# Kernel optimization log

Hardware: AMD Instinct MI355X
Metric: run time of the kernel (lower is better)

The kernel has to match this reference:

```python
import jax, jax.numpy as jnp
import numpy as np

B, S, HID = 2, 2048, 2048
H, KV, D = 16, 8, 128          # query heads, kv heads, head dim
NREP = H // KV
EPS = 1e-6
THETA = 1000000.0
SCALE = 1.0 / np.sqrt(D)


def setup_inputs() -> dict:
    key = jax.random.key(0)
    ks = jax.random.split(key, 5)
    x = jax.random.normal(ks[0], (B, S, HID), jnp.float32)
    std = 0.02
    Wq = jax.random.normal(ks[1], (HID, H * D), jnp.float32) * std
    Wk = jax.random.normal(ks[2], (HID, KV * D), jnp.float32) * std
    Wv = jax.random.normal(ks[3], (HID, KV * D), jnp.float32) * std
    Wo = jax.random.normal(ks[4], (H * D, HID), jnp.float32) * std
    q_norm_w = jnp.ones((D,), jnp.float32)
    k_norm_w = jnp.ones((D,), jnp.float32)
    # standard RoPE cos/sin table: [S, D]
    inv_freq = 1.0 / (THETA ** (jnp.arange(0, D, 2, dtype=jnp.float32) / D))
    freqs = jnp.arange(S, dtype=jnp.float32)[:, None] * inv_freq[None, :]
    emb = jnp.concatenate([freqs, freqs], axis=-1)
    return {"x": x, "Wq": Wq, "Wk": Wk, "Wv": Wv, "Wo": Wo,
            "q_norm_w": q_norm_w, "k_norm_w": k_norm_w,
            "cos": jnp.cos(emb), "sin": jnp.sin(emb)}


def _rmsnorm(x, w, eps=EPS):
    var = jnp.mean(jnp.square(x), axis=-1, keepdims=True)
    return w * (x * jax.lax.rsqrt(var + eps))


def _rotate_half(x):
    x1, x2 = jnp.split(x, 2, axis=-1)
    return jnp.concatenate([-x2, x1], axis=-1)


def _rope(t, cos, sin):
    # t: [B, h, S, D]; cos/sin: [S, D]
    return t * cos[None, None] + _rotate_half(t) * sin[None, None]


def reference(x, Wq, Wk, Wv, Wo, q_norm_w, k_norm_w, cos, sin):
    q = (x @ Wq).reshape(B, S, H, D)
    k = (x @ Wk).reshape(B, S, KV, D)
    v = (x @ Wv).reshape(B, S, KV, D)
    q = _rmsnorm(q, q_norm_w).transpose(0, 2, 1, 3)   # [B, H, S, D]
    k = _rmsnorm(k, k_norm_w).transpose(0, 2, 1, 3)   # [B, KV, S, D]
    v = v.transpose(0, 2, 1, 3)                       # [B, KV, S, D]
    q = _rope(q, cos, sin)
    k = _rope(k, cos, sin)
    # GQA without materializing repeated K/V: group q heads per kv head
    qg = q.reshape(B, KV, NREP, S, D)
    scores = jnp.einsum('bgrsd,bgtd->bgrst', qg, k) * SCALE  # [B,KV,NREP,S,S]
    causal = jnp.tril(jnp.ones((S, S), dtype=bool))
    scores = jnp.where(causal, scores, jnp.finfo(scores.dtype).min)
    p = jax.nn.softmax(scores, axis=-1)
    out = jnp.einsum('bgrst,bgtd->bgrsd', p, v).reshape(B, H, S, D)
    out = out.transpose(0, 2, 1, 3).reshape(B, S, H * D)
    return out @ Wo
```

## Files before the change

kernel.cpp:

```cpp
#include <hip/hip_runtime.h>

typedef unsigned short u16;
typedef __bf16 bf16x8 __attribute__((ext_vector_type(8)));
typedef float f32x4 __attribute__((ext_vector_type(4)));

#define Bn 2
#define Sn 2048
#define HIDn 2048
#define Hn 16
#define KVn 8
#define Dn 128
#define SCALEf 0.08838834764831845f

__device__ __forceinline__ float b2f(u16 v) {
  return __builtin_bit_cast(float, (unsigned)v << 16);
}
__device__ __forceinline__ u16 f2b(float f) {
  unsigned u = __builtin_bit_cast(unsigned, f);
  u += 0x7fffu + ((u >> 16) & 1u);
  return (u16)(u >> 16);
}
__device__ __forceinline__ bool is_bf16(const void* det) {
  return *(const unsigned*)det == 0x3F803F80u;
}
__device__ __forceinline__ float ldx(const void* p, long i, bool isbf) {
  return isbf ? b2f(((const u16*)p)[i]) : ((const float*)p)[i];
}
__device__ __forceinline__ void gl_lds16(const u16* g, u16* l) {
  __builtin_amdgcn_global_load_lds(
      (unsigned int __attribute__((address_space(1)))*)g,
      (unsigned int __attribute__((address_space(3)))*)l, 16, 0, 0);
}

template <int CTRL>
__device__ __forceinline__ float dpp_mov(float x) {
  return __builtin_bit_cast(
      float, __builtin_amdgcn_update_dpp(0, __builtin_bit_cast(int, x), CTRL,
                                         0xF, 0xF, true));
}
__device__ __forceinline__ float red16_max(float x) {
  x = fmaxf(x, dpp_mov<0xB1>(x));
  x = fmaxf(x, dpp_mov<0x4E>(x));
  x = fmaxf(x, dpp_mov<0x141>(x));
  x = fmaxf(x, dpp_mov<0x140>(x));
  return x;
}
__device__ __forceinline__ float red16_sum(float x) {
  x += dpp_mov<0xB1>(x);
  x += dpp_mov<0x4E>(x);
  x += dpp_mov<0x141>(x);
  x += dpp_mov<0x140>(x);
  return x;
}

__global__ __launch_bounds__(256) void convert_x(
    const void* __restrict__ in, u16* __restrict__ out, const void* __restrict__ det) {
  bool isbf = is_bf16(det);
  long i = ((long)blockIdx.x * 256 + threadIdx.x) * 4;
  if (isbf) {
    *(ushort4*)(out + i) = *(const ushort4*)((const u16*)in + i);
  } else {
    float4 f = *(const float4*)((const float*)in + i);
    out[i] = f2b(f.x); out[i + 1] = f2b(f.y); out[i + 2] = f2b(f.z); out[i + 3] = f2b(f.w);
  }
}

__global__ __launch_bounds__(256) void transpose_any(
    const void* __restrict__ vin, u16* __restrict__ out, const void* __restrict__ det,
    int irs, int ors, long ib0, long ob0, int nb1, long ib1, long ob1) {
  __shared__ u16 tile[64][65];
  bool isbf = det ? is_bf16(det) : true;
  int bz = blockIdx.z;
  long ibase = (long)(bz / nb1) * ib0 + (long)(bz % nb1) * ib1;
  u16* op = out + (long)(bz / nb1) * ob0 + (long)(bz % nb1) * ob1;
  long r0 = (long)blockIdx.y * 64, c0 = (long)blockIdx.x * 64;
  int t = threadIdx.x;
  int tr = t >> 3, tc = (t & 7) * 8;
#pragma unroll
  for (int p = 0; p < 2; ++p) {
    int r = p * 32 + tr;
    long src = ibase + (r0 + r) * irs + c0 + tc;
    if (isbf) {
      const u16* ip = (const u16*)vin;
#pragma unroll
      for (int j = 0; j < 8; ++j) tile[r][tc + j] = ip[src + j];
    } else {
      const float* ip = (const float*)vin;
#pragma unroll
      for (int j = 0; j < 8; ++j) tile[r][tc + j] = f2b(ip[src + j]);
    }
  }
  __syncthreads();
#pragma unroll
  for (int p = 0; p < 2; ++p) {
    int r = p * 32 + tr;
    u16* dst = op + (c0 + r) * ors + r0 + tc;
#pragma unroll
    for (int j = 0; j < 8; ++j) dst[j] = tile[tc + j][r];
  }
}

__global__ __launch_bounds__(256) void gemm_bt(
    const u16* __restrict__ A, const u16* __restrict__ Bt, u16* __restrict__ C,
    float* __restrict__ Cf, const void* __restrict__ det, int N, int K) {
  __shared__ alignas(16) u16 As[128 * 64];
  __shared__ alignas(16) u16 Bs[128 * 64];
  int t = threadIdx.x;
  int wave = t >> 6, lane = t & 63, quad = lane >> 4, l15 = lane & 15;
  long bm = (long)blockIdx.y * 128, bn = (long)blockIdx.x * 128;
  int wm = (wave >> 1) * 64, wn = (wave & 1) * 64;
  f32x4 acc[4][4] = {};
  int sg = ((t & 7) ^ ((t >> 3) & 7)) * 8;
  const u16* Ab = A + (bm + (t >> 3)) * K + sg;
  const u16* Bb = Bt + (bn + (t >> 3)) * K + sg;
  for (int k0 = 0; k0 < K; k0 += 64) {
    __syncthreads();
#pragma unroll
    for (int p = 0; p < 4; ++p) {
      gl_lds16(Ab + (long)(p * 32) * K + k0, As + p * 2048 + t * 8);
      gl_lds16(Bb + (long)(p * 32) * K + k0, Bs + p * 2048 + t * 8);
    }
    __syncthreads();
#pragma unroll
    for (int kt = 0; kt < 2; ++kt) {
      int fg = ((kt * 4 + quad) ^ (l15 & 7)) * 8;
      bf16x8 a[4], b[4];
#pragma unroll
      for (int i = 0; i < 4; ++i)
        a[i] = *(const bf16x8*)(As + (wm + i * 16 + l15) * 64 + fg);
#pragma unroll
      for (int j = 0; j < 4; ++j)
        b[j] = *(const bf16x8*)(Bs + (wn + j * 16 + l15) * 64 + fg);
#pragma unroll
      for (int i = 0; i < 4; ++i)
#pragma unroll
        for (int j = 0; j < 4; ++j)
          acc[i][j] = __builtin_amdgcn_mfma_f32_16x16x32_bf16(a[i], b[j], acc[i][j], 0, 0, 0);
    }
  }
  bool tofloat = (Cf != nullptr) && !is_bf16(det);
#pragma unroll
  for (int i = 0; i < 4; ++i) {
    long row = bm + wm + i * 16 + quad * 4;
#pragma unroll
    for (int j = 0; j < 4; ++j) {
      long col = bn + wn + j * 16 + l15;
      if (tofloat) {
#pragma unroll
        for (int r = 0; r < 4; ++r) Cf[(row + r) * N + col] = acc[i][j][r];
      } else {
#pragma unroll
        for (int r = 0; r < 4; ++r) C[(row + r) * N + col] = f2b(acc[i][j][r]);
      }
    }
  }
}

__global__ __launch_bounds__(256) void gemm_qkv(
    const u16* __restrict__ A, const u16* __restrict__ Bt,
    u16* __restrict__ Qout, u16* __restrict__ Kout, u16* __restrict__ Vout,
    int hq, int hk,
    const void* __restrict__ qw, const void* __restrict__ kw,
    const void* __restrict__ cosb, const void* __restrict__ sinb, int K) {
  __shared__ alignas(16) u16 As[128 * 64];
  __shared__ alignas(16) u16 Bs[128 * 64];
  bool isbf = is_bf16(qw);
  int t = threadIdx.x;
  int wave = t >> 6, lane = t & 63, quad = lane >> 4, l15 = lane & 15;
  long bm = (long)blockIdx.y * 128;
  int h = blockIdx.x;
  long bn = (long)h * 128;
  int wm = wave * 32;
  f32x4 acc[2][8] = {};
  int sg = ((t & 7) ^ ((t >> 3) & 7)) * 8;
  const u16* Ab = A + (bm + (t >> 3)) * K + sg;
  const u16* Bb = Bt + (bn + (t >> 3)) * K + sg;
  for (int k0 = 0; k0 < K; k0 += 64) {
    __syncthreads();
#pragma unroll
    for (int p = 0; p < 4; ++p) {
      gl_lds16(Ab + (long)(p * 32) * K + k0, As + p * 2048 + t * 8);
      gl_lds16(Bb + (long)(p * 32) * K + k0, Bs + p * 2048 + t * 8);
    }
    __syncthreads();
#pragma unroll
    for (int kt = 0; kt < 2; ++kt) {
      int fg = ((kt * 4 + quad) ^ (l15 & 7)) * 8;
      bf16x8 a[2], b[8];
#pragma unroll
      for (int i = 0; i < 2; ++i)
        a[i] = *(const bf16x8*)(As + (wm + i * 16 + l15) * 64 + fg);
#pragma unroll
      for (int j = 0; j < 8; ++j)
        b[j] = *(const bf16x8*)(Bs + (j * 16 + l15) * 64 + fg);
#pragma unroll
      for (int i = 0; i < 2; ++i)
#pragma unroll
        for (int j = 0; j < 8; ++j)
          acc[i][j] = __builtin_amdgcn_mfma_f32_16x16x32_bf16(a[i], b[j], acc[i][j], 0, 0, 0);
    }
  }
  if (h < hq + hk) {
    bool isq = h < hq;
    const void* w = isq ? qw : kw;
    int nh = isq ? Hn : KVn;
    int hh = isq ? h : (h - hq);
    u16* Obase = isq ? Qout : Kout;
#pragma unroll
    for (int i = 0; i < 2; ++i) {
#pragma unroll
      for (int r = 0; r < 4; ++r) {
        float ss = 0.f;
#pragma unroll
        for (int j = 0; j < 8; ++j) { float v = acc[i][j][r]; ss += v * v; }
        ss = red16_sum(ss);
        float scale = rsqrtf(ss * (1.0f / 128.0f) + 1e-6f);
        int m = (int)bm + wm + i * 16 + quad * 4 + r;
        int b = m >> 11, s = m & (Sn - 1);
        u16* dst = Obase + (((long)b * nh + hh) * Sn + s) * Dn;
        long cb = (long)s * Dn;
#pragma unroll
        for (int j = 0; j < 4; ++j) {
          int c1i = j * 16 + l15, c2i = c1i + 64;
          float x1 = acc[i][j][r] * scale * ldx(w, c1i, isbf);
          float x2 = acc[i][j + 4][r] * scale * ldx(w, c2i, isbf);
          float c1 = ldx(cosb, cb + c1i, isbf), s1 = ldx(sinb, cb + c1i, isbf);
          float c2 = ldx(cosb, cb + c2i, isbf), s2 = ldx(sinb, cb + c2i, isbf);
          dst[c1i] = f2b(x1 * c1 - x2 * s1);
          dst[c2i] = f2b(x2 * c2 + x1 * s2);
        }
      }
    }
  } else {
    int kv = h - hq - hk;
    int bidx = (int)(bm >> 11);
    int srow = ((int)bm & (Sn - 1)) + wm + quad * 4;
#pragma unroll
    for (int i = 0; i < 2; ++i) {
      int s0 = srow + i * 16;
#pragma unroll
      for (int j = 0; j < 8; ++j) {
        int d = j * 16 + l15;
        ushort4 tmp;
        tmp.x = f2b(acc[i][j][0]);
        tmp.y = f2b(acc[i][j][1]);
        tmp.z = f2b(acc[i][j][2]);
        tmp.w = f2b(acc[i][j][3]);
        *(ushort4*)(Vout + (((long)bidx * KVn + kv) * Dn + d) * Sn + s0) = tmp;
      }
    }
  }
}

__global__ __launch_bounds__(512) void attn_kernel(
    const u16* __restrict__ Qr, const u16* __restrict__ Kr,
    const u16* __restrict__ Vt, u16* __restrict__ Aout) {
  __shared__ alignas(16) u16 Ks[64 * 128];
  __shared__ alignas(16) u16 Vs[128 * 64];
  __shared__ alignas(16) u16 Ps[8][16 * 64];
  int t = threadIdx.x, wave = t >> 6, lane = t & 63, quad = lane >> 4, l15 = lane & 15;
  int bh = blockIdx.y, b = bh >> 4, h = bh & 15, kvh = h >> 1;
  const u16* kbase = Kr + ((long)b * KVn + kvh) * Sn * Dn;
  const u16* vbase = Vt + ((long)b * KVn + kvh) * (long)Dn * Sn;
  int krow = t >> 4;
  int kgr = ((t & 15) ^ (krow & 15)) * 8;
  int vrow = t >> 3;
  int vgr = ((t & 7) ^ (vrow & 7)) * 8;
  u16* ps = (u16*)Ps[wave];

  for (int half = 0; half < 2; ++half) {
    int qt = half == 0 ? (int)blockIdx.x : 15 - (int)blockIdx.x;
    int row0 = qt * 128 + wave * 16;
    const u16* qbase = Qr + (((long)b * Hn + h) * Sn + row0) * Dn;
    bf16x8 aq[4];
#pragma unroll
    for (int kt = 0; kt < 4; ++kt)
      aq[kt] = *(const bf16x8*)(qbase + l15 * Dn + kt * 32 + quad * 8);
    f32x4 o[8] = {};
    float mi[4], li[4];
#pragma unroll
    for (int r = 0; r < 4; ++r) { mi[r] = -1e30f; li[r] = 0.f; }
    int kv_end = qt * 128 + 128;
    for (int kv0 = 0; kv0 < kv_end; kv0 += 64) {
      __syncthreads();
      {
        const u16* kg = kbase + ((long)kv0 + krow) * Dn + kgr;
        gl_lds16(kg, Ks + t * 8);
        gl_lds16(kg + (long)32 * Dn, Ks + 4096 + t * 8);
        const u16* vg = vbase + (long)vrow * Sn + kv0 + vgr;
        gl_lds16(vg, Vs + t * 8);
        gl_lds16(vg + (long)64 * Sn, Vs + 4096 + t * 8);
      }
      __syncthreads();
      if (kv0 <= row0 + 15) {
        f32x4 sc[4] = {};
#pragma unroll
        for (int kt = 0; kt < 4; ++kt) {
          bf16x8 bk[4];
#pragma unroll
          for (int n = 0; n < 4; ++n)
            bk[n] = *(const bf16x8*)(Ks + (n * 16 + l15) * 128 + (((kt * 4 + quad) ^ l15) * 8));
#pragma unroll
          for (int n = 0; n < 4; ++n)
            sc[n] = __builtin_amdgcn_mfma_f32_16x16x32_bf16(aq[kt], bk[n], sc[n], 0, 0, 0);
        }
        f32x4 sv[4];
#pragma unroll
        for (int n = 0; n < 4; ++n)
#pragma unroll
          for (int r = 0; r < 4; ++r) sv[n][r] = sc[n][r] * SCALEf;
        if (kv0 + 63 > row0) {
#pragma unroll
          for (int n = 0; n < 4; ++n) {
            int col = kv0 + n * 16 + l15;
#pragma unroll
            for (int r = 0; r < 4; ++r)
              if (col > row0 + quad * 4 + r) sv[n][r] = -1e30f;
          }
        }
        float alpha[4], pr[4][4];
#pragma unroll
        for (int r = 0; r < 4; ++r) {
          float mx = fmaxf(fmaxf(sv[0][r], sv[1][r]), fmaxf(sv[2][r], sv[3][r]));
          mx = red16_max(mx);
          float mnew = fmaxf(mi[r], mx);
          alpha[r] = __expf(mi[r] - mnew);
          mi[r] = mnew;
          float rs = 0.f;
#pragma unroll
          for (int n = 0; n < 4; ++n) {
            float pv = __expf(sv[n][r] - mnew);
            pr[r][n] = pv;
            rs += pv;
          }
          rs = red16_sum(rs);
          li[r] = li[r] * alpha[r] + rs;
        }
#pragma unroll
        for (int n = 0; n < 8; ++n)
#pragma unroll
          for (int r = 0; r < 4; ++r) o[n][r] *= alpha[r];
#pragma unroll
        for (int n = 0; n < 4; ++n)
#pragma unroll
          for (int r = 0; r < 4; ++r) {
            int prow = quad * 4 + r;
            int pg = (n * 2 + (l15 >> 3)) ^ (prow & 7);
            ps[prow * 64 + pg * 8 + (l15 & 7)] = f2b(pr[r][n]);
          }
#pragma unroll
        for (int kt2 = 0; kt2 < 2; ++kt2) {
          bf16x8 ap = *(const bf16x8*)(ps + l15 * 64 + (((kt2 * 4 + quad) ^ (l15 & 7)) * 8));
#pragma unroll
          for (int n = 0; n < 8; ++n) {
            bf16x8 bv = *(const bf16x8*)(Vs + (n * 16 + l15) * 64 + (((kt2 * 4 + quad) ^ (l15 & 7)) * 8));
            o[n] = __builtin_amdgcn_mfma_f32_16x16x32_bf16(ap, bv, o[n], 0, 0, 0);
          }
        }
      }
    }
#pragma unroll
    for (int r = 0; r < 4; ++r) {
      long s = row0 + quad * 4 + r;
      float inv = 1.0f / li[r];
      u16* dst = Aout + (((long)b * Sn + s) * Hn + h) * Dn;
#pragma unroll
      for (int n = 0; n < 8; ++n) dst[n * 16 + l15] = f2b(o[n][r] * inv);
    }
  }
}

extern "C" void kernel_launch(void* const* d_in, const int* in_sizes, int n_in,
                              void* d_out, int out_size, void* d_ws, size_t ws_size,
                              hipStream_t stream) {
  (void)in_sizes; (void)n_in; (void)out_size;
  const void* x    = d_in[0];
  const void* Wq   = d_in[1];
  const void* Wk   = d_in[2];
  const void* Wv   = d_in[3];
  const void* Wo   = d_in[4];
  const void* qw   = d_in[5];
  const void* kw   = d_in[6];
  const void* cosb = d_in[7];
  const void* sinb = d_in[8];
  u16* ws = (u16*)d_ws;
  u16* dsc = (u16*)d_out;

  u16* Qr = dsc + 0;
  u16* Kr = dsc + 8388608;
  u16* xb = ws + 0;
  dim3 blk(256);
  convert_x<<<dim3(8192), blk, 0, stream>>>(x, xb, qw);

  if (ws_size >= (size_t)33554432) {
    u16* WT = ws + 8388608;
    u16* Vt = dsc + 12582912;
    transpose_any<<<dim3(32, 32, 1), blk, 0, stream>>>(Wq, WT, qw, 2048, 2048, 0, 0, 1, 0, 0);
    transpose_any<<<dim3(16, 32, 1), blk, 0, stream>>>(Wk, WT + (long)2048 * 2048, qw, 1024, 2048, 0, 0, 1, 0, 0);
    transpose_any<<<dim3(16, 32, 1), blk, 0, stream>>>(Wv, WT + (long)3072 * 2048, qw, 1024, 2048, 0, 0, 1, 0, 0);
    gemm_qkv<<<dim3(32, 32), blk, 0, stream>>>(xb, WT, Qr, Kr, Vt, Hn, KVn,
                                               qw, kw, cosb, sinb, 2048);
    u16* attn = ws + 0;
    attn_kernel<<<dim3(8, 32), dim3(512), 0, stream>>>(Qr, Kr, Vt, attn);
    u16* WoT = ws + 8388608;
    transpose_any<<<dim3(32, 32, 1), blk, 0, stream>>>(Wo, WoT, qw, 2048, 2048, 0, 0, 1, 0, 0);
    gemm_bt<<<dim3(16, 32), blk, 0, stream>>>(attn, WoT, (u16*)d_out, (float*)d_out, qw, 2048, 2048);
  } else {
    u16* Wslot = dsc + 12582912;
    u16* Vt    = ws + 8388608;
    transpose_any<<<dim3(32, 32, 1), blk, 0, stream>>>(Wq, Wslot, qw, 2048, 2048, 0, 0, 1, 0, 0);
    gemm_qkv<<<dim3(16, 32), blk, 0, stream>>>(xb, Wslot, Qr, nullptr, nullptr, Hn, 0,
                                               qw, kw, cosb, sinb, 2048);
    transpose_any<<<dim3(16, 32, 1), blk, 0, stream>>>(Wk, Wslot, qw, 1024, 2048, 0, 0, 1, 0, 0);
    transpose_any<<<dim3(16, 32, 1), blk, 0, stream>>>(Wv, Wslot + (long)1024 * 2048, qw, 1024, 2048, 0, 0, 1, 0, 0);
    gemm_qkv<<<dim3(16, 32), blk, 0, stream>>>(xb, Wslot, nullptr, Kr, Vt, 0, KVn,
                                               qw, kw, cosb, sinb, 2048);
    u16* attn = ws + 0;
    attn_kernel<<<dim3(8, 32), dim3(512), 0, stream>>>(Qr, Kr, Vt, attn);
    u16* WoT = ws + 8388608;
    transpose_any<<<dim3(32, 32, 1), blk, 0, stream>>>(Wo, WoT, qw, 2048, 2048, 0, 0, 1, 0, 0);
    gemm_bt<<<dim3(16, 32), blk, 0, stream>>>(attn, WoT, (u16*)d_out, (float*)d_out, qw, 2048, 2048);
  }
}
```

Baseline: 371.3 us.

## Rewrite QKV GEMM as 256x256 tile with double-buffered LDS pipeline

Replaces the 128x128, 256-thread QKV projection GEMM with a 256x256-tile, 512-thread kernel. It double-buffers A and B tiles in LDS, issues next-tile global loads between MFMA phases, and raises wave priority around MFMA bursts. The aim is to raise data reuse per tile and hide global-load latency behind compute. It uses far more LDS and registers per block and launches only 256 blocks, which risks occupancy and CU balance. The small-workspace fallback path is removed, so the kernel now assumes the workspace is large enough.

Result: faster. 360.9 us (-2.8%).

```diff
diff --git a/kernel.cpp b/kernel.cpp
--- a/kernel.cpp
+++ b/kernel.cpp
@@ -156,74 +156,146 @@
   }
 }
 
-__global__ __launch_bounds__(256) void gemm_qkv(
+__global__ __launch_bounds__(512, 2) void gemm_qkv256(
     const u16* __restrict__ A, const u16* __restrict__ Bt,
     u16* __restrict__ Qout, u16* __restrict__ Kout, u16* __restrict__ Vout,
-    int hq, int hk,
     const void* __restrict__ qw, const void* __restrict__ kw,
     const void* __restrict__ cosb, const void* __restrict__ sinb, int K) {
-  __shared__ alignas(16) u16 As[128 * 64];
-  __shared__ alignas(16) u16 Bs[128 * 64];
+  __shared__ alignas(16) u16 As[2][2][8192];
+  __shared__ alignas(16) u16 Bs[2][2][8192];
+  const int NT = K >> 6;
   bool isbf = is_bf16(qw);
   int t = threadIdx.x;
   int wave = t >> 6, lane = t & 63, quad = lane >> 4, l15 = lane & 15;
-  long bm = (long)blockIdx.y * 128;
-  int h = blockIdx.x;
-  long bn = (long)h * 128;
-  int wm = wave * 32;
-  f32x4 acc[2][8] = {};
-  int sg = ((t & 7) ^ ((t >> 3) & 7)) * 8;
-  const u16* Ab = A + (bm + (t >> 3)) * K + sg;
-  const u16* Bb = Bt + (bn + (t >> 3)) * K + sg;
-  for (int k0 = 0; k0 < K; k0 += 64) {
-    __syncthreads();
-#pragma unroll
-    for (int p = 0; p < 4; ++p) {
-      gl_lds16(Ab + (long)(p * 32) * K + k0, As + p * 2048 + t * 8);
-      gl_lds16(Bb + (long)(p * 32) * K + k0, Bs + p * 2048 + t * 8);
-    }
-    __syncthreads();
-#pragma unroll
-    for (int kt = 0; kt < 2; ++kt) {
-      int fg = ((kt * 4 + quad) ^ (l15 & 7)) * 8;
-      bf16x8 a[2], b[8];
-#pragma unroll
-      for (int i = 0; i < 2; ++i)
-        a[i] = *(const bf16x8*)(As + (wm + i * 16 + l15) * 64 + fg);
-#pragma unroll
-      for (int j = 0; j < 8; ++j)
-        b[j] = *(const bf16x8*)(Bs + (j * 16 + l15) * 64 + fg);
-#pragma unroll
-      for (int i = 0; i < 2; ++i)
-#pragma unroll
-        for (int j = 0; j < 8; ++j)
-          acc[i][j] = __builtin_amdgcn_mfma_f32_16x16x32_bf16(a[i], b[j], acc[i][j], 0, 0, 0);
-    }
-  }
-  if (h < hq + hk) {
-    bool isq = h < hq;
+  int l7 = l15 & 7;
+  int wmi = wave >> 1, wni = wave & 1;
+  long bm = (long)blockIdx.y * 256;
+  long bn = (long)blockIdx.x * 256;
+  int s0 = t, s1 = t + 512;
+  int r0 = s0 >> 3, r1 = s1 >> 3;
+  int gs0 = (s0 & 7) ^ (r0 & 7), gs1 = (s1 & 7) ^ (r1 & 7);
+  const u16* Ab0 = A + bm * K;
+  const u16* Ab1 = A + (bm + 128) * K;
+  const u16* Bb0 = Bt + bn * K;
+  const u16* Bb1 = Bt + (bn + 128) * K;
+#define STG(dst, src)                                          \
+  gl_lds16((src) + (long)r0 * K + gs0 * 8, (dst) + s0 * 8);    \
+  gl_lds16((src) + (long)r1 * K + gs1 * 8, (dst) + s1 * 8);
+#define FENCE asm volatile("" ::: "memory")
+  int ah = wmi >> 1;
+  int arb = (wmi & 1) * 64 + l15;
+#define LDA(m, kk) (*(const bf16x8*)(Ah + (arb + (m)*16) * 64 + ((((kk)*4 + quad) ^ l7) * 8)))
+#define LDB(n, kk) (*(const bf16x8*)(Bh + ((n)*16 + l15) * 64 + ((((kk)*4 + quad) ^ l7) * 8)))
+  f32x4 acc[4][8] = {};
+  STG((u16*)As[0][0], Ab0);
+  STG((u16*)As[0][1], Ab1);
+  STG((u16*)Bs[0][0], Bb0);
+  STG((u16*)Bs[0][1], Bb1);
+  STG((u16*)As[1][0], Ab0 + 64);
+  STG((u16*)As[1][1], Ab1 + 64);
+  asm volatile("s_waitcnt vmcnt(4)" ::: "memory");
+  __builtin_amdgcn_s_barrier();
+
+  for (int tk = 0; tk < NT; ++tk) {
+    const u16* Ah = (const u16*)As[tk & 1][ah];
+    const u16* Bh = (const u16*)Bs[tk & 1][wni];
+    u16* BsN0 = (u16*)Bs[(tk + 1) & 1][0];
+    u16* BsN1 = (u16*)Bs[(tk + 1) & 1][1];
+    u16* AsN0 = (u16*)As[tk & 1][0];
+    u16* AsN1 = (u16*)As[tk & 1][1];
+    bf16x8 aa[4], bb[4];
+#pragma unroll
+    for (int m = 0; m < 4; ++m) aa[m] = LDA(m, 0);
+#pragma unroll
+    for (int j = 0; j < 4; ++j) bb[j] = LDB(j, 0);
+    if (tk + 1 < NT) { STG(BsN0, Bb0 + (tk + 1) * 64); }
+    FENCE; __builtin_amdgcn_s_barrier();
+    asm volatile("s_waitcnt lgkmcnt(0)" ::: "memory");
+    __builtin_amdgcn_s_setprio(1);
+#pragma unroll
+    for (int m = 0; m < 4; ++m)
+#pragma unroll
+      for (int j = 0; j < 4; ++j)
+        acc[m][j] = __builtin_amdgcn_mfma_f32_16x16x32_bf16(aa[m], bb[j], acc[m][j], 0, 0, 0);
+    __builtin_amdgcn_s_setprio(0);
+    FENCE; __builtin_amdgcn_s_barrier();
+#pragma unroll
+    for (int j = 0; j < 4; ++j) bb[j] = LDB(j + 4, 0);
+    if (tk + 1 < NT) { STG(BsN1, Bb1 + (tk + 1) * 64); }
+    FENCE; __builtin_amdgcn_s_barrier();
+    asm volatile("s_waitcnt lgkmcnt(0)" ::: "memory");
+    __builtin_amdgcn_s_setprio(1);
+#pragma unroll
+    for (int m = 0; m < 4; ++m)
+#pragma unroll
+      for (int j = 0; j < 4; ++j)
+        acc[m][j + 4] = __builtin_amdgcn_mfma_f32_16x16x32_bf16(aa[m], bb[j], acc[m][j + 4], 0, 0, 0);
+    __builtin_amdgcn_s_setprio(0);
+    FENCE; __builtin_amdgcn_s_barrier();
+#pragma unroll
+    for (int m = 0; m < 4; ++m) aa[m] = LDA(m, 1);
+#pragma unroll
+    for (int j = 0; j < 4; ++j) bb[j] = LDB(j, 1);
+    FENCE; __builtin_amdgcn_s_barrier();
+    asm volatile("s_waitcnt lgkmcnt(0)" ::: "memory");
+    __builtin_amdgcn_s_setprio(1);
+#pragma unroll
+    for (int m = 0; m < 4; ++m)
+#pragma unroll
+      for (int j = 0; j < 4; ++j)
+        acc[m][j] = __builtin_amdgcn_mfma_f32_16x16x32_bf16(aa[m], bb[j], acc[m][j], 0, 0, 0);
+    __builtin_amdgcn_s_setprio(0);
+    FENCE; __builtin_amdgcn_s_barrier();
+#pragma unroll
+    for (int j = 0; j < 4; ++j) bb[j] = LDB(j + 4, 1);
+    if (tk + 2 < NT) {
+      STG(AsN0, Ab0 + (tk + 2) * 64);
+      STG(AsN1, Ab1 + (tk + 2) * 64);
+      asm volatile("s_waitcnt vmcnt(4)" ::: "memory");
+    } else {
+      asm volatile("s_waitcnt vmcnt(0)" ::: "memory");
+    }
+    __builtin_amdgcn_s_barrier();
+    asm volatile("s_waitcnt lgkmcnt(0)" ::: "memory");
+    __builtin_amdgcn_s_setprio(1);
+#pragma unroll
+    for (int m = 0; m < 4; ++m)
+#pragma unroll
+      for (int j = 0; j < 4; ++j)
+        acc[m][j + 4] = __builtin_amdgcn_mfma_f32_16x16x32_bf16(aa[m], bb[j], acc[m][j + 4], 0, 0, 0);
+    __builtin_amdgcn_s_setprio(0);
+    FENCE; __builtin_amdgcn_s_barrier();
+  }
+#undef STG
+#undef LDA
+#undef LDB
+#undef FENCE
+  int hglob = (int)(bn >> 7) + wni;
+  int mrow0 = (int)bm + wmi * 64 + quad * 4;
+  if (hglob < Hn + KVn) {
+    bool isq = hglob < Hn;
     const void* w = isq ? qw : kw;
     int nh = isq ? Hn : KVn;
-    int hh = isq ? h : (h - hq);
-    u16* Obase = isq ? Qout : Kout;
-#pragma unroll
-    for (int i = 0; i < 2; ++i) {
+    int hh = isq ? hglob : hglob - Hn;
+    u16* Ob = isq ? Qout : Kout;
+#pragma unroll
+    for (int m = 0; m < 4; ++m) {
 #pragma unroll
       for (int r = 0; r < 4; ++r) {
         float ss = 0.f;
 #pragma unroll
-        for (int j = 0; j < 8; ++j) { float v = acc[i][j][r]; ss += v * v; }
+        for (int j = 0; j < 8; ++j) { float v = acc[m][j][r]; ss += v * v; }
         ss = red16_sum(ss);
         float scale = rsqrtf(ss * (1.0f / 128.0f) + 1e-6f);
-        int m = (int)bm + wm + i * 16 + quad * 4 + r;
-        int b = m >> 11, s = m & (Sn - 1);
-        u16* dst = Obase + (((long)b * nh + hh) * Sn + s) * Dn;
+        int mr = mrow0 + m * 16 + r;
+        int b = mr >> 11, s = mr & (Sn - 1);
+        u16* dst = Ob + (((long)b * nh + hh) * Sn + s) * Dn;
         long cb = (long)s * Dn;
 #pragma unroll
         for (int j = 0; j < 4; ++j) {
           int c1i = j * 16 + l15, c2i = c1i + 64;
-          float x1 = acc[i][j][r] * scale * ldx(w, c1i, isbf);
-          float x2 = acc[i][j + 4][r] * scale * ldx(w, c2i, isbf);
+          float x1 = acc[m][j][r] * scale * ldx(w, c1i, isbf);
+          float x2 = acc[m][j + 4][r] * scale * ldx(w, c2i, isbf);
           float c1 = ldx(cosb, cb + c1i, isbf), s1 = ldx(sinb, cb + c1i, isbf);
           float c2 = ldx(cosb, cb + c2i, isbf), s2 = ldx(sinb, cb + c2i, isbf);
           dst[c1i] = f2b(x1 * c1 - x2 * s1);
@@ -232,21 +304,21 @@
       }
     }
   } else {
-    int kv = h - hq - hk;
+    int kv = hglob - Hn - KVn;
     int bidx = (int)(bm >> 11);
-    int srow = ((int)bm & (Sn - 1)) + wm + quad * 4;
-#pragma unroll
-    for (int i = 0; i < 2; ++i) {
-      int s0 = srow + i * 16;
+    int srow = ((int)bm & (Sn - 1)) + wmi * 64 + quad * 4;
+#pragma unroll
+    for (int m = 0; m < 4; ++m) {
+      int sb = srow + m * 16;
 #pragma unroll
       for (int j = 0; j < 8; ++j) {
         int d = j * 16 + l15;
         ushort4 tmp;
-        tmp.x = f2b(acc[i][j][0]);
-        tmp.y = f2b(acc[i][j][1]);
-        tmp.z = f2b(acc[i][j][2]);
-        tmp.w = f2b(acc[i][j][3]);
-        *(ushort4*)(Vout + (((long)bidx * KVn + kv) * Dn + d) * Sn + s0) = tmp;
+        tmp.x = f2b(acc[m][j][0]);
+        tmp.y = f2b(acc[m][j][1]);
+        tmp.z = f2b(acc[m][j][2]);
+        tmp.w = f2b(acc[m][j][3]);
+        *(ushort4*)(Vout + (((long)bidx * KVn + kv) * Dn + d) * Sn + sb) = tmp;
       }
     }
   }
@@ -373,7 +445,7 @@
 extern "C" void kernel_launch(void* const* d_in, const int* in_sizes, int n_in,
                               void* d_out, int out_size, void* d_ws, size_t ws_size,
                               hipStream_t stream) {
-  (void)in_sizes; (void)n_in; (void)out_size;
+  (void)in_sizes; (void)n_in; (void)out_size; (void)ws_size;
   const void* x    = d_in[0];
   const void* Wq   = d_in[1];
   const void* Wk   = d_in[2];
@@ -388,37 +460,19 @@
 
   u16* Qr = dsc + 0;
   u16* Kr = dsc + 8388608;
+  u16* Vt = dsc + 12582912;
   u16* xb = ws + 0;
+  u16* WT = ws + 8388608;
   dim3 blk(256);
   convert_x<<<dim3(8192), blk, 0, stream>>>(x, xb, qw);
-
-  if (ws_size >= (size_t)33554432) {
-    u16* WT = ws + 8388608;
-    u16* Vt = dsc + 12582912;
-    transpose_any<<<dim3(32, 32, 1), blk, 0, stream>>>(Wq, WT, qw, 2048, 2048, 0, 0, 1, 0, 0);
-    transpose_any<<<dim3(16, 32, 1), blk, 0, stream>>>(Wk, WT + (long)2048 * 2048, qw, 1024, 2048, 0, 0, 1, 0, 0);
-    transpose_any<<<dim3(16, 32, 1), blk, 0, stream>>>(Wv, WT + (long)3072 * 2048, qw, 1024, 2048, 0, 0, 1, 0, 0);
-    gemm_qkv<<<dim3(32, 32), blk, 0, stream>>>(xb, WT, Qr, Kr, Vt, Hn, KVn,
-                                               qw, kw, cosb, sinb, 2048);
-    u16* attn = ws + 0;
-    attn_kernel<<<dim3(8, 32), dim3(512), 0, stream>>>(Qr, Kr, Vt, attn);
-    u16* WoT = ws + 8388608;
-    transpose_any<<<dim3(32, 32, 1), blk, 0, stream>>>(Wo, WoT, qw, 2048, 2048, 0, 0, 1, 0, 0);
-    gemm_bt<<<dim3(16, 32), blk, 0, stream>>>(attn, WoT, (u16*)d_out, (float*)d_out, qw, 2048, 2048);
-  } else {
-    u16* Wslot = dsc + 12582912;
-    u16* Vt    = ws + 8388608;
-    transpose_any<<<dim3(32, 32, 1), blk, 0, stream>>>(Wq, Wslot, qw, 2048, 2048, 0, 0, 1, 0, 0);
-    gemm_qkv<<<dim3(16, 32), blk, 0, stream>>>(xb, Wslot, Qr, nullptr, nullptr, Hn, 0,
-                                               qw, kw, cosb, sinb, 2048);
-    transpose_any<<<dim3(16, 32, 1), blk, 0, stream>>>(Wk, Wslot, qw, 1024, 2048, 0, 0, 1, 0, 0);
-    transpose_any<<<dim3(16, 32, 1), blk, 0, stream>>>(Wv, Wslot + (long)1024 * 2048, qw, 1024, 2048, 0, 0, 1, 0, 0);
-    gemm_qkv<<<dim3(16, 32), blk, 0, stream>>>(xb, Wslot, nullptr, Kr, Vt, 0, KVn,
-                                               qw, kw, cosb, sinb, 2048);
-    u16* attn = ws + 0;
-    attn_kernel<<<dim3(8, 32), dim3(512), 0, stream>>>(Qr, Kr, Vt, attn);
-    u16* WoT = ws + 8388608;
-    transpose_any<<<dim3(32, 32, 1), blk, 0, stream>>>(Wo, WoT, qw, 2048, 2048, 0, 0, 1, 0, 0);
-    gemm_bt<<<dim3(16, 32), blk, 0, stream>>>(attn, WoT, (u16*)d_out, (float*)d_out, qw, 2048, 2048);
-  }
-}
+  transpose_any<<<dim3(32, 32, 1), blk, 0, stream>>>(Wq, WT, qw, 2048, 2048, 0, 0, 1, 0, 0);
+  transpose_any<<<dim3(16, 32, 1), blk, 0, stream>>>(Wk, WT + (long)2048 * 2048, qw, 1024, 2048, 0, 0, 1, 0, 0);
+  transpose_any<<<dim3(16, 32, 1), blk, 0, stream>>>(Wv, WT + (long)3072 * 2048, qw, 1024, 2048, 0, 0, 1, 0, 0);
+  gemm_qkv256<<<dim3(16, 16), dim3(512), 0, stream>>>(xb, WT, Qr, Kr, Vt,
+                                                      qw, kw, cosb, sinb, 2048);
+  u16* attn = ws + 0;
+  attn_kernel<<<dim3(8, 32), dim3(512), 0, stream>>>(Qr, Kr, Vt, attn);
+  u16* WoT = ws + 8388608;
+  transpose_any<<<dim3(32, 32, 1), blk, 0, stream>>>(Wo, WoT, qw, 2048, 2048, 0, 0, 1, 0, 0);
+  gemm_bt<<<dim3(16, 32), blk, 0, stream>>>(attn, WoT, (u16*)d_out, (float*)d_out, qw, 2048, 2048);
+}
```
